# Performance work log

Hardware: AMD Instinct MI355X
Metric: run time of the kernel (lower is better)

Reference implementation:

```python
import jax, jax.numpy as jnp
import numpy as np

N = 50000      # num nodes (== num segments for aggregation)
E = 800000     # num edges
D_IN = 128
D_OUT = 128


def setup_inputs() -> dict:
    key = jax.random.key(0)
    k1, k2, k3, k4, k5, k6 = jax.random.split(key, 6)
    x = jax.random.normal(k1, (N, D_IN), dtype=jnp.float32)
    edge_rows = jax.random.randint(k2, (E,), 0, N, dtype=jnp.int32)
    edge_cols = jax.random.randint(k3, (E,), 0, N, dtype=jnp.int32)
    edge_vals = jax.random.uniform(k4, (E,), dtype=jnp.float32)
    stdv = 1.0 / np.sqrt(D_OUT)
    weight = jax.random.uniform(k5, (D_IN, D_OUT), dtype=jnp.float32, minval=-stdv, maxval=stdv)
    root_weight = jax.random.uniform(k6, (D_IN, D_OUT), dtype=jnp.float32, minval=-stdv, maxval=stdv)
    return {"x": x, "edge_rows": edge_rows, "edge_cols": edge_cols,
            "edge_vals": edge_vals, "weight": weight, "root_weight": root_weight}


def reference(x, edge_rows, edge_cols, edge_vals, weight, root_weight):
    # support = x @ W                                  [N, D_OUT]
    support = jnp.dot(x, weight)
    # out = spmm(adj, support): adj in COO form.
    # message per edge: adj[r, c] * support[c]         [E, D_OUT]
    msgs = support[edge_cols] * edge_vals[:, None]
    agg = jax.ops.segment_sum(msgs, edge_rows, num_segments=N)  # [N, D_OUT]
    # out += x @ W_root  (bias=False configuration)
    return agg + jnp.dot(x, root_weight)
```

## Files before the change

kernel.cpp:

```cpp
#include <hip/hip_runtime.h>

#define D 128
#define NC 128
#define RPB 128
#define MAXBUCK 512

typedef short short8 __attribute__((ext_vector_type(8)));
typedef float v4f __attribute__((ext_vector_type(4)));

static __device__ __forceinline__ unsigned short f2bf(float f) {
    unsigned u = __builtin_bit_cast(unsigned, f);
    u = (u + 0x7FFFu + ((u >> 16) & 1u)) >> 16;
    return (unsigned short)u;
}

__global__ __launch_bounds__(256) void bucket_hist_prep(
    const int* __restrict__ rows, int* __restrict__ countsT,
    const float* __restrict__ W, const float* __restrict__ Wr,
    unsigned short* __restrict__ Wt, int E, int nbuck, int chunk)
{
    __shared__ int hist[MAXBUCK];
    const int t = threadIdx.x, c = blockIdx.x;
    {
        const int gid = c * 256 + t;
        const int k  = gid >> 8;
        const int nn = gid & 255;
        const float v = (nn < D) ? W[k * D + nn] : Wr[k * D + (nn - D)];
        Wt[nn * D + k] = f2bf(v);
    }
    for (int i = t; i < nbuck; i += 256) hist[i] = 0;
    __syncthreads();
    const int base = c * chunk;
    const int endv = min(base + chunk, E);
    for (int e = base + t; e < endv; e += 256)
        atomicAdd(&hist[__builtin_nontemporal_load(rows + e) >> 7], 1);
    __syncthreads();
    for (int i = t; i < nbuck; i += 256) countsT[i * NC + c] = hist[i];
}

__global__ __launch_bounds__(256) void gemm_dual_mfma(
    const float* __restrict__ x, const unsigned short* __restrict__ Wt,
    unsigned short* __restrict__ support, float* __restrict__ out, int M)
{
    __shared__ unsigned short As[64][136];
    const int tid = threadIdx.x;
    const int w = tid >> 6;
    const int lane = tid & 63;
    const int nl = lane & 15, quad = lane >> 4;
    const int rowBase = blockIdx.x * 64;

    {
        const int r = tid & 63;
        const int seg = tid >> 6;
        const int row = rowBase + r;
        unsigned short tmp[32];
        if (row < M) {
            const float4* src = (const float4*)(x + (size_t)row * D + seg * 32);
            #pragma unroll
            for (int j = 0; j < 8; ++j) {
                const float4 v = src[j];
                tmp[j * 4 + 0] = f2bf(v.x); tmp[j * 4 + 1] = f2bf(v.y);
                tmp[j * 4 + 2] = f2bf(v.z); tmp[j * 4 + 3] = f2bf(v.w);
            }
        } else {
            #pragma unroll
            for (int j = 0; j < 32; ++j) tmp[j] = 0;
        }
        #pragma unroll
        for (int j = 0; j < 4; ++j)
            *(short8*)&As[r][seg * 32 + j * 8] = *(const short8*)&tmp[j * 8];
    }

    short8 bfrag[4][4];
    {
        const unsigned short* wbase = Wt + (size_t)(w * 64 + nl) * D + quad * 8;
        #pragma unroll
        for (int nt = 0; nt < 4; ++nt)
            #pragma unroll
            for (int c = 0; c < 4; ++c)
                bfrag[c][nt] = *(const short8*)(wbase + (size_t)nt * 16 * D + c * 32);
    }
    __syncthreads();

    v4f acc[4][4] = {};
    #pragma unroll
    for (int c = 0; c < 4; ++c) {
        short8 afr[4];
        #pragma unroll
        for (int mt = 0; mt < 4; ++mt)
            afr[mt] = *(const short8*)&As[mt * 16 + nl][c * 32 + quad * 8];
        #pragma unroll
        for (int mt = 0; mt < 4; ++mt)
            #pragma unroll
            for (int nt = 0; nt < 4; ++nt)
                acc[mt][nt] = __builtin_amdgcn_mfma_f32_16x16x32_bf16(
                    afr[mt], bfrag[c][nt], acc[mt][nt], 0, 0, 0);
    }

    const int cbase = (w & 1) * 64;
    if (w < 2) {
        #pragma unroll
        for (int mt = 0; mt < 4; ++mt)
            #pragma unroll
            for (int reg = 0; reg < 4; ++reg) {
                const int row = rowBase + mt * 16 + quad * 4 + reg;
                if (row < M) {
                    #pragma unroll
                    for (int nt = 0; nt < 4; ++nt)
                        support[(size_t)row * D + cbase + nt * 16 + nl] = f2bf(acc[mt][nt][reg]);
                }
            }
    } else {
        #pragma unroll
        for (int mt = 0; mt < 4; ++mt)
            #pragma unroll
            for (int reg = 0; reg < 4; ++reg) {
                const int row = rowBase + mt * 16 + quad * 4 + reg;
                if (row < M) {
                    #pragma unroll
                    for (int nt = 0; nt < 4; ++nt)
                        out[(size_t)row * D + cbase + nt * 16 + nl] = acc[mt][nt][reg];
                }
            }
    }
}

__global__ __launch_bounds__(256) void scan_local(
    const int* __restrict__ counts, int* __restrict__ eoff,
    int* __restrict__ block_sums, int n)
{
    __shared__ int tmp[256];
    const int b = blockIdx.x, t = threadIdx.x;
    const int base = b * 1024 + t * 4;
    int v0 = 0, v1 = 0, v2 = 0, v3 = 0;
    if (base + 3 < n) {
        const int4 q = *(const int4*)(counts + base);
        v0 = q.x; v1 = q.y; v2 = q.z; v3 = q.w;
    } else {
        if (base + 0 < n) v0 = counts[base + 0];
        if (base + 1 < n) v1 = counts[base + 1];
        if (base + 2 < n) v2 = counts[base + 2];
    }
    const int s01 = v0 + v1;
    const int tsum = s01 + v2 + v3;
    tmp[t] = tsum;
    __syncthreads();
    for (int off = 1; off < 256; off <<= 1) {
        const int u = (t >= off) ? tmp[t - off] : 0;
        __syncthreads();
        tmp[t] += u;
        __syncthreads();
    }
    const int excl = tmp[t] - tsum;
    const int e0 = excl, e1 = excl + v0, e2 = excl + s01, e3 = e2 + v2;
    if (base + 3 < n) {
        *(int4*)(eoff + base) = make_int4(e0, e1, e2, e3);
    } else {
        if (base + 0 < n) eoff[base + 0] = e0;
        if (base + 1 < n) eoff[base + 1] = e1;
        if (base + 2 < n) eoff[base + 2] = e2;
    }
    if (t == 255) block_sums[b] = tmp[255];
}

__global__ __launch_bounds__(256) void add_offsets(
    const int* __restrict__ block_sums, int* __restrict__ eoff, int n, int nb)
{
    __shared__ int sb[64];
    const int b = blockIdx.x, t = threadIdx.x;
    if (t < 64) sb[t] = (t < nb) ? block_sums[t] : 0;
    __syncthreads();
    int off = 0, tot = 0;
    for (int i = 0; i < nb; ++i) {
        const int v = sb[i];
        if (i < b) off += v;
        tot += v;
    }
    const int base = b * 1024 + t * 4;
    if (base + 3 < n) {
        int4 q = *(const int4*)(eoff + base);
        q.x += off; q.y += off; q.z += off; q.w += off;
        *(int4*)(eoff + base) = q;
    } else {
        #pragma unroll
        for (int j = 0; j < 4; ++j) {
            const int i = base + j;
            if (i < n) eoff[i] += off;
        }
    }
    if (b == nb - 1 && t == 0) eoff[n] = tot;
}

__global__ __launch_bounds__(256) void bucket_scatter(
    const int* __restrict__ rows, const int* __restrict__ cols,
    const float* __restrict__ vals, const int* __restrict__ eoff,
    int2* __restrict__ sortedB, int E, int nbuck, int chunk)
{
    __shared__ int cur[MAXBUCK];
    const int t = threadIdx.x, c = blockIdx.x;
    for (int i = t; i < nbuck; i += 256) cur[i] = eoff[i * NC + c];
    __syncthreads();
    const int base = c * chunk;
    const int endv = min(base + chunk, E);
    for (int e = base + t; e < endv; e += 256) {
        const int r  = __builtin_nontemporal_load(rows + e);
        const int cl = __builtin_nontemporal_load(cols + e);
        const float v = __builtin_nontemporal_load(vals + e);
        const int bk = r >> 7;
        const int pos = atomicAdd(&cur[bk], 1);
        sortedB[pos] = make_int2(((r & (RPB - 1)) << 16) | cl, __float_as_int(v));
    }
}

__global__ __launch_bounds__(256) void bucket_sort(
    const int* __restrict__ eoff, const int2* __restrict__ sortedB,
    int2* __restrict__ sortedF, int* __restrict__ row_start, int nbuck)
{
    __shared__ int hist[RPB];
    __shared__ int scn[RPB];
    const int b = blockIdx.x, t = threadIdx.x;
    const int base = eoff[b * NC];
    const int endv = eoff[(b + 1) * NC];
    if (t < RPB) hist[t] = 0;
    __syncthreads();
    for (int i = base + t; i < endv; i += 256)
        atomicAdd(&hist[sortedB[i].x >> 16], 1);
    __syncthreads();
    if (t < RPB) scn[t] = hist[t];
    __syncthreads();
    for (int off = 1; off < RPB; off <<= 1) {
        const int u = (t < RPB && t >= off) ? scn[t - off] : 0;
        __syncthreads();
        if (t < RPB) scn[t] += u;
        __syncthreads();
    }
    if (t < RPB) {
        const int ex = base + scn[t] - hist[t];
        row_start[b * RPB + t] = ex;
        hist[t] = ex;
    }
    __syncthreads();
    for (int i = base + t; i < endv; i += 256) {
        const int2 ed = sortedB[i];
        const int rib = ed.x >> 16;
        const int pos = atomicAdd(&hist[rib], 1);
        sortedF[pos] = make_int2(ed.x & 0xFFFF, ed.y);
    }
}

__global__ __launch_bounds__(256) void row_aggregate(
    const int* __restrict__ row_start, const int2* __restrict__ sorted,
    const unsigned short* __restrict__ support, float* __restrict__ out, int N)
{
    const int row = blockIdx.x * 4 + (threadIdx.x >> 6);
    const int lane = threadIdx.x & 63;
    if (row >= N) return;
    const int s = row_start[row];
    const int e = row_start[row + 1];
    if (s == e) return;

    float ax = 0.f, ay = 0.f;
    int i = s;

    for (; i + 16 <= e; i += 16) {
        int4 q[8];
        #pragma unroll
        for (int j = 0; j < 8; ++j) q[j] = *(const int4*)(sorted + i + 2 * j);
        int c[16], vv[16];
        #pragma unroll
        for (int j = 0; j < 8; ++j) {
            c[2 * j]     = q[j].x; vv[2 * j]     = q[j].y;
            c[2 * j + 1] = q[j].z; vv[2 * j + 1] = q[j].w;
        }
        unsigned p[16];
        #pragma unroll
        for (int j = 0; j < 16; ++j)
            p[j] = *(const unsigned*)(support + (size_t)c[j] * D + lane * 2);
        #pragma unroll
        for (int j = 0; j < 16; ++j) {
            const float v = __int_as_float(vv[j]);
            ax += __builtin_bit_cast(float, p[j] << 16) * v;
            ay += __builtin_bit_cast(float, p[j] & 0xFFFF0000u) * v;
        }
    }

    if (i + 8 <= e) {
        const int4 q0 = *(const int4*)(sorted + i + 0);
        const int4 q1 = *(const int4*)(sorted + i + 2);
        const int4 q2 = *(const int4*)(sorted + i + 4);
        const int4 q3 = *(const int4*)(sorted + i + 6);
        const int  c[8] = {q0.x, q0.z, q1.x, q1.z, q2.x, q2.z, q3.x, q3.z};
        const int  vv[8] = {q0.y, q0.w, q1.y, q1.w, q2.y, q2.w, q3.y, q3.w};
        unsigned p[8];
        #pragma unroll
        for (int j = 0; j < 8; ++j)
            p[j] = *(const unsigned*)(support + (size_t)c[j] * D + lane * 2);
        #pragma unroll
        for (int j = 0; j < 8; ++j) {
            const float v = __int_as_float(vv[j]);
            ax += __builtin_bit_cast(float, p[j] << 16) * v;
            ay += __builtin_bit_cast(float, p[j] & 0xFFFF0000u) * v;
        }
        i += 8;
    }

    if (i < e) {
        const int m = e - i;
        int cc[8]; float vv[8];
        #pragma unroll
        for (int j = 0; j < 8; ++j) {
            const int idx = i + (j < m ? j : m - 1);
            const int2 ed = sorted[idx];
            cc[j] = ed.x;
            vv[j] = (j < m) ? __int_as_float(ed.y) : 0.f;
        }
        unsigned p[8];
        #pragma unroll
        for (int j = 0; j < 8; ++j)
            p[j] = *(const unsigned*)(support + (size_t)cc[j] * D + lane * 2);
        #pragma unroll
        for (int j = 0; j < 8; ++j) {
            ax += __builtin_bit_cast(float, p[j] << 16) * vv[j];
            ay += __builtin_bit_cast(float, p[j] & 0xFFFF0000u) * vv[j];
        }
    }

    float* o = out + (size_t)row * D + lane * 2;
    float2 ov = *(const float2*)o;
    ov.x += ax;
    ov.y += ay;
    *(float2*)o = ov;
}

extern "C" void kernel_launch(void* const* d_in, const int* in_sizes, int n_in,
                              void* d_out, int out_size, void* d_ws, size_t ws_size,
                              hipStream_t stream) {
    const float* x     = (const float*)d_in[0];
    const int*   erows = (const int*)d_in[1];
    const int*   ecols = (const int*)d_in[2];
    const float* evals = (const float*)d_in[3];
    const float* W     = (const float*)d_in[4];
    const float* Wr    = (const float*)d_in[5];
    float* out = (float*)d_out;

    const int M = in_sizes[0] / D;
    const int E = in_sizes[1];

    const int nbuck = (M + RPB - 1) / RPB;
    const int n = nbuck * NC;
    const int chunk = (E + NC - 1) / NC;

    unsigned short* support = (unsigned short*)d_ws;
    unsigned short* Wt      = support + (size_t)M * D;
    int*   countsT    = (int*)(Wt + 2 * D * D);
    int*   eoff       = countsT + n;
    int*   block_sums = eoff + n + 2;
    int*   row_start  = block_sums + 64;
    int2*  sortedB    = (int2*)(row_start + nbuck * RPB + 2);
    int2*  sortedF    = sortedB + E;

    const int NB = (n + 1023) / 1024;

    bucket_hist_prep<<<NC, 256, 0, stream>>>(erows, countsT, W, Wr, Wt, E, nbuck, chunk);
    gemm_dual_mfma<<<(M + 63) / 64, 256, 0, stream>>>(x, Wt, support, out, M);
    scan_local<<<NB, 256, 0, stream>>>(countsT, eoff, block_sums, n);
    add_offsets<<<NB, 256, 0, stream>>>(block_sums, eoff, n, NB);
    bucket_scatter<<<NC, 256, 0, stream>>>(erows, ecols, evals, eoff, sortedB, E, nbuck, chunk);
    bucket_sort<<<nbuck, 256, 0, stream>>>(eoff, sortedB, sortedF, row_start, nbuck);
    row_aggregate<<<(M + 3) / 4, 256, 0, stream>>>(row_start, sortedF, support, out, M);
}
```

Before: 183.2 us.

## Pack edges into 32-bit words, store root product in bf16, double histogram chunks

Sorted edges become one 32-bit word each, holding a bf16 edge value and a 16-bit column index, which halves edge traffic in the aggregation kernel. The root GEMM result is now written as bf16 to a scratch buffer and added in row_aggregate, which also writes every output row once with a nontemporal store instead of a read-modify-write of out. NC goes from 128 to 256 to give the histogram and scatter kernels more parallelism. Risks: the 16-bit column index only holds because N=50000 is below 65536, and bf16 edge values and root output lower accuracy.

```diff
diff --git a/kernel.cpp b/kernel.cpp
--- a/kernel.cpp
+++ b/kernel.cpp
@@ -1,12 +1,14 @@
 #include <hip/hip_runtime.h>
 
 #define D 128
-#define NC 128
+#define NC 256
 #define RPB 128
 #define MAXBUCK 512
 
 typedef short short8 __attribute__((ext_vector_type(8)));
 typedef float v4f __attribute__((ext_vector_type(4)));
+typedef unsigned uint4v __attribute__((ext_vector_type(4)));
+typedef float float2v __attribute__((ext_vector_type(2)));
 
 static __device__ __forceinline__ unsigned short f2bf(float f) {
     unsigned u = __builtin_bit_cast(unsigned, f);
@@ -21,8 +23,8 @@
 {
     __shared__ int hist[MAXBUCK];
     const int t = threadIdx.x, c = blockIdx.x;
-    {
-        const int gid = c * 256 + t;
+    if (t < 128) {
+        const int gid = c * 128 + t;
         const int k  = gid >> 8;
         const int nn = gid & 255;
         const float v = (nn < D) ? W[k * D + nn] : Wr[k * D + (nn - D)];
@@ -40,7 +42,8 @@
 
 __global__ __launch_bounds__(256) void gemm_dual_mfma(
     const float* __restrict__ x, const unsigned short* __restrict__ Wt,
-    unsigned short* __restrict__ support, float* __restrict__ out, int M)
+    unsigned short* __restrict__ support, unsigned short* __restrict__ rootbuf,
+    int M)
 {
     __shared__ unsigned short As[64][136];
     const int tid = threadIdx.x;
@@ -98,31 +101,18 @@
     }
 
     const int cbase = (w & 1) * 64;
-    if (w < 2) {
-        #pragma unroll
-        for (int mt = 0; mt < 4; ++mt)
-            #pragma unroll
-            for (int reg = 0; reg < 4; ++reg) {
-                const int row = rowBase + mt * 16 + quad * 4 + reg;
-                if (row < M) {
-                    #pragma unroll
-                    for (int nt = 0; nt < 4; ++nt)
-                        support[(size_t)row * D + cbase + nt * 16 + nl] = f2bf(acc[mt][nt][reg]);
-                }
+    unsigned short* dst = (w < 2) ? support : rootbuf;
+    #pragma unroll
+    for (int mt = 0; mt < 4; ++mt)
+        #pragma unroll
+        for (int reg = 0; reg < 4; ++reg) {
+            const int row = rowBase + mt * 16 + quad * 4 + reg;
+            if (row < M) {
+                #pragma unroll
+                for (int nt = 0; nt < 4; ++nt)
+                    dst[(size_t)row * D + cbase + nt * 16 + nl] = f2bf(acc[mt][nt][reg]);
             }
-    } else {
-        #pragma unroll
-        for (int mt = 0; mt < 4; ++mt)
-            #pragma unroll
-            for (int reg = 0; reg < 4; ++reg) {
-                const int row = rowBase + mt * 16 + quad * 4 + reg;
-                if (row < M) {
-                    #pragma unroll
-                    for (int nt = 0; nt < 4; ++nt)
-                        out[(size_t)row * D + cbase + nt * 16 + nl] = acc[mt][nt][reg];
-                }
-            }
-    }
+        }
 }
 
 __global__ __launch_bounds__(256) void scan_local(
@@ -166,9 +156,9 @@
 __global__ __launch_bounds__(256) void add_offsets(
     const int* __restrict__ block_sums, int* __restrict__ eoff, int n, int nb)
 {
-    __shared__ int sb[64];
+    __shared__ int sb[128];
     const int b = blockIdx.x, t = threadIdx.x;
-    if (t < 64) sb[t] = (t < nb) ? block_sums[t] : 0;
+    if (t < 128) sb[t] = (t < nb) ? block_sums[t] : 0;
     __syncthreads();
     int off = 0, tot = 0;
     for (int i = 0; i < nb; ++i) {
@@ -214,7 +204,7 @@
 
 __global__ __launch_bounds__(256) void bucket_sort(
     const int* __restrict__ eoff, const int2* __restrict__ sortedB,
-    int2* __restrict__ sortedF, int* __restrict__ row_start, int nbuck)
+    unsigned* __restrict__ sortedF, int* __restrict__ row_start, int nbuck)
 {
     __shared__ int hist[RPB];
     __shared__ int scn[RPB];
@@ -244,60 +234,60 @@
         const int2 ed = sortedB[i];
         const int rib = ed.x >> 16;
         const int pos = atomicAdd(&hist[rib], 1);
-        sortedF[pos] = make_int2(ed.x & 0xFFFF, ed.y);
+        const unsigned vb = f2bf(__int_as_float(ed.y));
+        sortedF[pos] = (vb << 16) | (unsigned)(ed.x & 0xFFFF);
     }
 }
 
 __global__ __launch_bounds__(256) void row_aggregate(
-    const int* __restrict__ row_start, const int2* __restrict__ sorted,
-    const unsigned short* __restrict__ support, float* __restrict__ out, int N)
+    const int* __restrict__ row_start, const unsigned* __restrict__ sorted,
+    const unsigned short* __restrict__ support,
+    const unsigned short* __restrict__ rootbuf,
+    float* __restrict__ out, int N)
 {
     const int row = blockIdx.x * 4 + (threadIdx.x >> 6);
     const int lane = threadIdx.x & 63;
     if (row >= N) return;
     const int s = row_start[row];
     const int e = row_start[row + 1];
-    if (s == e) return;
 
     float ax = 0.f, ay = 0.f;
     int i = s;
 
     for (; i + 16 <= e; i += 16) {
-        int4 q[8];
-        #pragma unroll
-        for (int j = 0; j < 8; ++j) q[j] = *(const int4*)(sorted + i + 2 * j);
-        int c[16], vv[16];
-        #pragma unroll
-        for (int j = 0; j < 8; ++j) {
-            c[2 * j]     = q[j].x; vv[2 * j]     = q[j].y;
-            c[2 * j + 1] = q[j].z; vv[2 * j + 1] = q[j].w;
+        uint4v q[4];
+        #pragma unroll
+        for (int j = 0; j < 4; ++j)
+            q[j] = __builtin_nontemporal_load((const uint4v*)(sorted + i) + j);
+        unsigned d[16];
+        #pragma unroll
+        for (int j = 0; j < 4; ++j) {
+            d[4 * j] = q[j].x; d[4 * j + 1] = q[j].y;
+            d[4 * j + 2] = q[j].z; d[4 * j + 3] = q[j].w;
         }
         unsigned p[16];
         #pragma unroll
         for (int j = 0; j < 16; ++j)
-            p[j] = *(const unsigned*)(support + (size_t)c[j] * D + lane * 2);
+            p[j] = *(const unsigned*)(support + (size_t)(d[j] & 0xFFFF) * D + lane * 2);
         #pragma unroll
         for (int j = 0; j < 16; ++j) {
-            const float v = __int_as_float(vv[j]);
+            const float v = __builtin_bit_cast(float, d[j] & 0xFFFF0000u);
             ax += __builtin_bit_cast(float, p[j] << 16) * v;
             ay += __builtin_bit_cast(float, p[j] & 0xFFFF0000u) * v;
         }
     }
 
     if (i + 8 <= e) {
-        const int4 q0 = *(const int4*)(sorted + i + 0);
-        const int4 q1 = *(const int4*)(sorted + i + 2);
-        const int4 q2 = *(const int4*)(sorted + i + 4);
-        const int4 q3 = *(const int4*)(sorted + i + 6);
-        const int  c[8] = {q0.x, q0.z, q1.x, q1.z, q2.x, q2.z, q3.x, q3.z};
-        const int  vv[8] = {q0.y, q0.w, q1.y, q1.w, q2.y, q2.w, q3.y, q3.w};
+        const uint4v q0 = __builtin_nontemporal_load((const uint4v*)(sorted + i));
+        const uint4v q1 = __builtin_nontemporal_load((const uint4v*)(sorted + i) + 1);
+        const unsigned d[8] = {q0.x, q0.y, q0.z, q0.w, q1.x, q1.y, q1.z, q1.w};
         unsigned p[8];
         #pragma unroll
         for (int j = 0; j < 8; ++j)
-            p[j] = *(const unsigned*)(support + (size_t)c[j] * D + lane * 2);
+            p[j] = *(const unsigned*)(support + (size_t)(d[j] & 0xFFFF) * D + lane * 2);
         #pragma unroll
         for (int j = 0; j < 8; ++j) {
-            const float v = __int_as_float(vv[j]);
+            const float v = __builtin_bit_cast(float, d[j] & 0xFFFF0000u);
             ax += __builtin_bit_cast(float, p[j] << 16) * v;
             ay += __builtin_bit_cast(float, p[j] & 0xFFFF0000u) * v;
         }
@@ -306,30 +296,30 @@
 
     if (i < e) {
         const int m = e - i;
-        int cc[8]; float vv[8];
+        unsigned d[8];
         #pragma unroll
         for (int j = 0; j < 8; ++j) {
             const int idx = i + (j < m ? j : m - 1);
-            const int2 ed = sorted[idx];
-            cc[j] = ed.x;
-            vv[j] = (j < m) ? __int_as_float(ed.y) : 0.f;
+            const unsigned q = sorted[idx];
+            d[j] = (j < m) ? q : (q & 0xFFFFu);
         }
         unsigned p[8];
         #pragma unroll
         for (int j = 0; j < 8; ++j)
-            p[j] = *(const unsigned*)(support + (size_t)cc[j] * D + lane * 2);
+            p[j] = *(const unsigned*)(support + (size_t)(d[j] & 0xFFFF) * D + lane * 2);
         #pragma unroll
         for (int j = 0; j < 8; ++j) {
-            ax += __builtin_bit_cast(float, p[j] << 16) * vv[j];
-            ay += __builtin_bit_cast(float, p[j] & 0xFFFF0000u) * vv[j];
-        }
-    }
-
-    float* o = out + (size_t)row * D + lane * 2;
-    float2 ov = *(const float2*)o;
-    ov.x += ax;
-    ov.y += ay;
-    *(float2*)o = ov;
+            const float v = __builtin_bit_cast(float, d[j] & 0xFFFF0000u);
+            ax += __builtin_bit_cast(float, p[j] << 16) * v;
+            ay += __builtin_bit_cast(float, p[j] & 0xFFFF0000u) * v;
+        }
+    }
+
+    const unsigned pr = *(const unsigned*)(rootbuf + (size_t)row * D + lane * 2);
+    float2v ov;
+    ov.x = ax + __builtin_bit_cast(float, pr << 16);
+    ov.y = ay + __builtin_bit_cast(float, pr & 0xFFFF0000u);
+    __builtin_nontemporal_store(ov, (float2v*)(out + (size_t)row * D + lane * 2));
 }
 
 extern "C" void kernel_launch(void* const* d_in, const int* in_sizes, int n_in,
@@ -352,20 +342,21 @@
 
     unsigned short* support = (unsigned short*)d_ws;
     unsigned short* Wt      = support + (size_t)M * D;
-    int*   countsT    = (int*)(Wt + 2 * D * D);
-    int*   eoff       = countsT + n;
-    int*   block_sums = eoff + n + 2;
-    int*   row_start  = block_sums + 64;
-    int2*  sortedB    = (int2*)(row_start + nbuck * RPB + 2);
-    int2*  sortedF    = sortedB + E;
+    unsigned short* rootbuf = Wt + 2 * D * D;
+    int*      countsT    = (int*)(rootbuf + (size_t)M * D);
+    int*      eoff       = countsT + n;
+    int*      block_sums = eoff + n + 2;
+    int*      row_start  = block_sums + 128;
+    int2*     sortedB    = (int2*)(row_start + nbuck * RPB + 2);
+    unsigned* sortedF    = (unsigned*)(sortedB + E);
 
     const int NB = (n + 1023) / 1024;
 
     bucket_hist_prep<<<NC, 256, 0, stream>>>(erows, countsT, W, Wr, Wt, E, nbuck, chunk);
-    gemm_dual_mfma<<<(M + 63) / 64, 256, 0, stream>>>(x, Wt, support, out, M);
+    gemm_dual_mfma<<<(M + 63) / 64, 256, 0, stream>>>(x, Wt, support, rootbuf, M);
     scan_local<<<NB, 256, 0, stream>>>(countsT, eoff, block_sums, n);
     add_offsets<<<NB, 256, 0, stream>>>(block_sums, eoff, n, NB);
     bucket_scatter<<<NC, 256, 0, stream>>>(erows, ecols, evals, eoff, sortedB, E, nbuck, chunk);
     bucket_sort<<<nbuck, 256, 0, stream>>>(eoff, sortedB, sortedF, row_start, nbuck);
-    row_aggregate<<<(M + 3) / 4, 256, 0, stream>>>(row_start, sortedF, support, out, M);
-}
+    row_aggregate<<<(M + 3) / 4, 256, 0, stream>>>(row_start, sortedF, support, rootbuf, out, M);
+}
```

Result: faster. 167.5 us (-8.6%).
